# Kernel optimization log

Hardware: AMD Instinct MI355X
Metric: run time of the kernel (lower is better)

The kernel has to match this reference:

```python
import jax, jax.numpy as jnp
import numpy as np

# dims
N, T = 16, 2000            # batch, encoder frames
ENC, DEC = 512, 512        # enc_dim, dec_dim
ATT, C, K, H = 512, 10, 64, 4  # att_dim, conv_channels, loc_context, att_head


def setup_inputs() -> dict:
    key = jax.random.key(0)
    ks = jax.random.split(key, 16)
    s = 0.02
    enc_pad = jax.random.normal(ks[0], (N, T, ENC), jnp.float32)
    enc_len = jax.random.randint(ks[1], (N,), T // 2, T + 1, jnp.int32)
    dec_prev = jax.random.normal(ks[2], (N, DEC), jnp.float32)
    ali_prev = jax.random.uniform(ks[3], (N, H, T), jnp.float32)
    ali_prev = ali_prev / ali_prev.sum(-1, keepdims=True)
    # parameters (torch layout)
    We = jax.random.normal(ks[4], (ATT * H, ENC), jnp.float32) * s   # enc_proj weight
    be = jnp.zeros((ATT * H,), jnp.float32)                          # enc_proj bias
    Wk = jax.random.normal(ks[5], (ATT * H, ENC), jnp.float32) * s   # key_proj
    Wd = jax.random.normal(ks[6], (ATT * H, DEC), jnp.float32) * s   # dec_proj
    WF = jax.random.normal(ks[7], (C * H, 1, 2 * K + 1), jnp.float32) * s  # F: grouped conv1d
    bF = jnp.zeros((C * H,), jnp.float32)
    Wa = jax.random.normal(ks[8], (H, ATT, C), jnp.float32) * s      # att: 1x1 grouped conv, per-head [ATT,C]
    Ww = jax.random.normal(ks[9], (H, ATT), jnp.float32) * s         # w: 1x1 grouped conv, per-head [ATT]
    Wc = jax.random.normal(ks[10], (ENC, ATT * H), jnp.float32) * s  # ctx_proj
    bc = jnp.zeros((ENC,), jnp.float32)
    return {"enc_pad": enc_pad, "enc_len": enc_len, "dec_prev": dec_prev,
            "ali_prev": ali_prev, "We": We, "be": be, "Wk": Wk, "Wd": Wd,
            "WF": WF, "bF": bF, "Wa": Wa, "Ww": Ww, "Wc": Wc, "bc": bc}


def reference(enc_pad, enc_len, dec_prev, ali_prev, We, be, Wk, Wd, WF, bF, Wa, Ww, Wc, bc):
    n, t, _ = enc_pad.shape
    # enc_part: N x H x T x D
    ep = enc_pad @ We.T + be
    enc_part = ep.reshape(n, t, H, ATT).transpose(0, 2, 1, 3)
    # key_part: N x H x D x T (matches torch transpose(1,2).view ordering)
    kp = enc_pad @ Wk.T
    key_part = kp.transpose(0, 2, 1).reshape(n, H, ATT, t)
    # pad mask: N x T, True where padded
    pad_mask = jnp.arange(t)[None, :] >= enc_len[:, None]
    # location features: grouped conv1d over alignment, per head
    f = jax.lax.conv_general_dilated(
        ali_prev, WF, window_strides=(1,), padding=[(K, K)],
        dimension_numbers=("NCH", "OIH", "NCH"), feature_group_count=H)
    f = (f + bF[None, :, None]).reshape(n, H, C, t)
    # 1x1 grouped conv: C -> ATT per head
    att_part = jnp.einsum("hdc,nhct->nhdt", Wa, f)
    dec_part = (dec_prev @ Wd.T).reshape(n, H, ATT)
    sum_part = jnp.tanh(att_part + key_part + dec_part[..., None])  # N x H x D x T
    score = jnp.einsum("hd,nhdt->nht", Ww, sum_part)                # N x H x T
    score = jnp.where(pad_mask[:, None, :], -jnp.inf, score)
    ali = jax.nn.softmax(score, axis=-1)
    ctx = jnp.einsum("nht,nhtd->nhd", ali, enc_part).reshape(n, H * ATT)
    ctx = ctx @ Wc.T + bc
    return ali, ctx
```

## Files before the change

### kernel.cpp

```cpp
#include <hip/hip_runtime.h>

#define NB   16
#define TT   2000
#define TP   2048
#define SPT  2048
#define ENC  512
#define ATTD 512
#define HH   4
#define CC   10
#define KK   64
#define KW   129
#define HATT 2048

typedef unsigned short u16;
typedef __attribute__((ext_vector_type(8))) short bf16x8;
typedef __attribute__((ext_vector_type(4))) float f32x4;

#define AS1 __attribute__((address_space(1)))
#define AS3 __attribute__((address_space(3)))

#define CVT_BLOCKS   2176
#define CVT_THREADS  (CVT_BLOCKS * 256)

__device__ inline unsigned bfpack2(float lo, float hi) {
    unsigned a = __builtin_bit_cast(unsigned, lo);
    unsigned b = __builtin_bit_cast(unsigned, hi);
    a = (a + 0x7fffu + ((a >> 16) & 1u)) >> 16;
    b = (b + 0x7fffu + ((b >> 16) & 1u)) >> 16;
    return a | (b << 16);
}

__global__ __launch_bounds__(256) void prep_kernel(
    const float* __restrict__ enc, const float* __restrict__ Wk,
    const float* __restrict__ ali_prev, const float* __restrict__ WF,
    const float* __restrict__ bF, const float* __restrict__ dec_prev,
    const float* __restrict__ Wd, const float* __restrict__ Wa,
    const int* __restrict__ enc_len,
    u16* __restrict__ Abf, u16* __restrict__ Wkbf,
    u16* __restrict__ ftb, u16* __restrict__ wab,
    float* __restrict__ decp)
{
    __shared__ union {
        struct { float aliW[632]; float wfT[KW * CC]; float bfs[CC]; } cv;
        float dsl[16 * 128];
    } sm;
    const int bid = blockIdx.x, tid = threadIdx.x;

    if (bid < CVT_BLOCKS) {
        const long long ATOT = (long long)NB * TP * ENC;
        f32x4 v[4][2];
        bool live[4];
        long long g[4];
        #pragma unroll
        for (int it = 0; it < 4; it++) {
            long long cid = (long long)it * CVT_THREADS + bid * 256 + tid;
            long long gid = cid * 8;
            g[it] = gid;
            const float* s;
            bool valid = true;
            if (gid < ATOT) {
                int n = (int)(gid >> 20);
                int rem = (int)(gid & ((1 << 20) - 1));
                int r = rem >> 9, e = rem & 511;
                valid = (r < enc_len[n]);
                s = enc + ((long long)n * TT + r) * ENC + e;
            } else {
                s = Wk + (gid - ATOT);
            }
            live[it] = valid;
            if (valid) {
                v[it][0] = __builtin_nontemporal_load((const f32x4*)s);
                v[it][1] = __builtin_nontemporal_load((const f32x4*)s + 1);
            }
        }
        #pragma unroll
        for (int it = 0; it < 4; it++) {
            if (!live[it]) continue;
            uint4 out;
            out.x = bfpack2(v[it][0].x, v[it][0].y);
            out.y = bfpack2(v[it][0].z, v[it][0].w);
            out.z = bfpack2(v[it][1].x, v[it][1].y);
            out.w = bfpack2(v[it][1].z, v[it][1].w);
            if (g[it] < ATOT) *(uint4*)(Abf + g[it]) = out;
            else              *(uint4*)(Wkbf + (g[it] - ATOT)) = out;
        }
    } else if (bid < CVT_BLOCKS + 256) {
        int b2 = bid - CVT_BLOCKS;
        int tc = b2 & 3, h = (b2 >> 2) & 3, n = b2 >> 4;
        int t0 = tc * 500;
        float* aliW = sm.cv.aliW;
        float* wfT  = sm.cv.wfT;
        float* bfs  = sm.cv.bfs;
        const float* arow = ali_prev + ((long long)n * HH + h) * TT;
        for (int i = tid; i < 632; i += 256) {
            int tt = t0 - KK + i;
            aliW[i] = (tt >= 0 && tt < TT) ? arow[tt] : 0.f;
        }
        for (int i = tid; i < KW * CC; i += 256) {
            int k = i / CC, c = i - k * CC;
            wfT[i] = WF[(h * CC + c) * KW + k];
        }
        if (tid < CC) bfs[tid] = bF[h * CC + tid];
        __syncthreads();
        if (tid < 250) {
            float acc0[CC], acc1[CC];
            #pragma unroll
            for (int c = 0; c < CC; c++) { acc0[c] = 0.f; acc1[c] = 0.f; }
            const int base = 2 * tid;
            float2 w0 = *(const float2*)&aliW[base];
            for (int k = 0; k < 128; k += 2) {
                float2 w2 = *(const float2*)&aliW[base + k + 2];
                #pragma unroll
                for (int cj = 0; cj < 5; cj++) {
                    float2 fk  = *(const float2*)&wfT[k * CC + cj * 2];
                    float2 fk1 = *(const float2*)&wfT[(k + 1) * CC + cj * 2];
                    acc0[2*cj]   += w0.x * fk.x + w0.y * fk1.x;
                    acc0[2*cj+1] += w0.x * fk.y + w0.y * fk1.y;
                    acc1[2*cj]   += w0.y * fk.x + w2.x * fk1.x;
                    acc1[2*cj+1] += w0.y * fk.y + w2.x * fk1.y;
                }
                w0 = w2;
            }
            #pragma unroll
            for (int cj = 0; cj < 5; cj++) {
                float2 fk = *(const float2*)&wfT[128 * CC + cj * 2];
                acc0[2*cj]   += w0.x * fk.x;  acc0[2*cj+1] += w0.x * fk.y;
                acc1[2*cj]   += w0.y * fk.x;  acc1[2*cj+1] += w0.y * fk.y;
            }
            #pragma unroll
            for (int c = 0; c < CC; c++) { acc0[c] += bfs[c]; acc1[c] += bfs[c]; }
            int t = t0 + base;
            u16* frow = ftb + (((long long)(n * HH + h)) * TP + t) * 16;
            uint4 ra, rb;
            ra.x = bfpack2(acc0[0], acc0[1]); ra.y = bfpack2(acc0[2], acc0[3]);
            ra.z = bfpack2(acc0[4], acc0[5]); ra.w = bfpack2(acc0[6], acc0[7]);
            rb.x = bfpack2(acc0[8], acc0[9]); rb.y = 0u; rb.z = 0u; rb.w = 0u;
            *(uint4*)(frow)     = ra; *(uint4*)(frow + 8)  = rb;
            ra.x = bfpack2(acc1[0], acc1[1]); ra.y = bfpack2(acc1[2], acc1[3]);
            ra.z = bfpack2(acc1[4], acc1[5]); ra.w = bfpack2(acc1[6], acc1[7]);
            rb.x = bfpack2(acc1[8], acc1[9]);
            *(uint4*)(frow + 16) = ra; *(uint4*)(frow + 24) = rb;
        } else if (tc == 3) {
            uint4 z = {0u, 0u, 0u, 0u};
            int r0 = 2000 + (tid - 250) * 8;
            u16* frow = ftb + (((long long)(n * HH + h)) * TP + r0) * 16;
            for (int r = 0; r < 8; r++) {
                *(uint4*)(frow + r * 16)     = z;
                *(uint4*)(frow + r * 16 + 8) = z;
            }
        }
    } else if (bid < CVT_BLOCKS + 288) {
        int b2 = bid - (CVT_BLOCKS + 256);
        int kc = b2 >> 3, jc = b2 & 7;
        for (int i = tid; i < 2048; i += 256) {
            int nn = i >> 7, kk = i & 127;
            sm.dsl[i] = dec_prev[nn * 512 + kc * 128 + kk];
        }
        __syncthreads();
        int d = jc * 256 + tid;
        float acc[NB];
        #pragma unroll
        for (int n = 0; n < NB; n++) acc[n] = 0.f;
        const float4* w4 = (const float4*)(Wd + (long long)d * 512 + kc * 128);
        for (int e4 = 0; e4 < 32; e4++) {
            float4 w = w4[e4];
            #pragma unroll
            for (int n = 0; n < NB; n++) {
                const float* a = sm.dsl + n * 128 + e4 * 4;
                acc[n] += w.x * a[0] + w.y * a[1] + w.z * a[2] + w.w * a[3];
            }
        }
        #pragma unroll
        for (int n = 0; n < NB; n++) decp[((long long)kc * NB + n) * HATT + d] = acc[n];
    } else {
        int b2 = bid - (CVT_BLOCKS + 288);
        int j0 = b2 * 512 + tid * 2;
        #pragma unroll
        for (int q = 0; q < 2; q++) {
            int j = j0 + q;
            int hh = j >> 9, dd = j & 511;
            const float* wr = Wa + ((long long)(hh * ATTD + dd)) * CC;
            uint4 ra, rb;
            ra.x = bfpack2(wr[0], wr[1]); ra.y = bfpack2(wr[2], wr[3]);
            ra.z = bfpack2(wr[4], wr[5]); ra.w = bfpack2(wr[6], wr[7]);
            rb.x = bfpack2(wr[8], wr[9]); rb.y = 0u; rb.z = 0u; rb.w = 0u;
            u16* out = wab + (long long)j * 16;
            *(uint4*)(out)     = ra;
            *(uint4*)(out + 8) = rb;
        }
    }
}

__global__ __launch_bounds__(256, 4) void score_gemm_kernel(
    const u16* __restrict__ Abf, const u16* __restrict__ Bbf,
    const u16* __restrict__ ftb, const u16* __restrict__ wab,
    const float* __restrict__ decp, const float* __restrict__ Ww,
    const int* __restrict__ enc_len, float* __restrict__ score_part)
{
    __shared__ __attribute__((aligned(16))) char smem[32768];
    float* sred = (float*)smem;

    const int bid = blockIdx.x;
    const int xcd = bid & 7;
    const int lcl = bid >> 3;
    const int nt = lcl & 15;
    const int rr = lcl >> 4;
    const int n = rr >> 1, half = rr & 1;
    const int mtl = (xcd + n) & 7;
    const int mt = half ? (8 + mtl) : mtl;

    if (mt * 128 >= enc_len[n]) return;

    const int tid = threadIdx.x, wave = tid >> 6, lane = tid & 63;
    const int l16 = lane & 15, lk = lane >> 4;
    const int h = nt >> 2;

    const u16* Aptr = Abf + ((long long)n * TP + mt * 128) * ENC;
    const u16* Bptr = Bbf + (long long)nt * 128 * ENC;

    f32x4 acc[4][4];
    #pragma unroll
    for (int mi = 0; mi < 4; mi++)
        #pragma unroll
        for (int nj = 0; nj < 4; nj++) {
            f32x4 z = {0.f, 0.f, 0.f, 0.f};
            acc[mi][nj] = z;
        }

    const int wrow = (wave >> 1) * 64, wcol = (wave & 1) * 64;
    const int t0 = mt * 128, dd0 = (nt & 3) * 128;

    for (int kt = 0; kt < 8; kt++) {
        const int k0 = kt * 64;
        #pragma unroll
        for (int i = 0; i < 4; i++) {
            int b = i * 4096 + tid * 16;
            int r = b >> 7, kb = b & 127;
            int kbs = kb ^ ((r & 7) << 4);
            __builtin_amdgcn_global_load_lds(
                (const AS1 void*)(Aptr + r * ENC + k0 + (kbs >> 1)),
                (AS3 void*)(smem + i * 4096 + wave * 1024), 16, 0, 0);
            __builtin_amdgcn_global_load_lds(
                (const AS1 void*)(Bptr + r * ENC + k0 + (kbs >> 1)),
                (AS3 void*)(smem + 16384 + i * 4096 + wave * 1024), 16, 0, 0);
        }
        __syncthreads();
        #pragma unroll
        for (int ks = 0; ks < 64; ks += 32) {
            bf16x8 af[4], bf[4];
            #pragma unroll
            for (int mi = 0; mi < 4; mi++) {
                int row = wrow + mi * 16 + l16;
                int cb = (ks * 2 + lk * 16) ^ ((row & 7) << 4);
                af[mi] = *(const bf16x8*)(smem + row * 128 + cb);
            }
            #pragma unroll
            for (int nj = 0; nj < 4; nj++) {
                int row = wcol + nj * 16 + l16;
                int cb = (ks * 2 + lk * 16) ^ ((row & 7) << 4);
                bf[nj] = *(const bf16x8*)(smem + 16384 + row * 128 + cb);
            }
            #pragma unroll
            for (int mi = 0; mi < 4; mi++)
                #pragma unroll
                for (int nj = 0; nj < 4; nj++)
                    acc[mi][nj] = __builtin_amdgcn_mfma_f32_16x16x32_bf16(
                        af[mi], bf[nj], acc[mi][nj], 0, 0, 0);
        }
        __syncthreads();
    }

    {
        bf16x8 zer = {0, 0, 0, 0, 0, 0, 0, 0};
        bf16x8 af[4], bf[4];
        #pragma unroll
        for (int mi = 0; mi < 4; mi++) af[mi] = zer;
        #pragma unroll
        for (int nj = 0; nj < 4; nj++) bf[nj] = zer;
        if (lk < 2) {
            #pragma unroll
            for (int mi = 0; mi < 4; mi++)
                af[mi] = *(const bf16x8*)(ftb +
                    (((long long)(n * HH + h)) * TP + t0 + wrow + mi * 16 + l16) * 16 + lk * 8);
            #pragma unroll
            for (int nj = 0; nj < 4; nj++)
                bf[nj] = *(const bf16x8*)(wab +
                    ((long long)(nt * 128 + wcol + nj * 16 + l16)) * 16 + lk * 8);
        }
        #pragma unroll
        for (int mi = 0; mi < 4; mi++)
            #pragma unroll
            for (int nj = 0; nj < 4; nj++)
                acc[mi][nj] = __builtin_amdgcn_mfma_f32_16x16x32_bf16(
                    af[mi], bf[nj], acc[mi][nj], 0, 0, 0);
    }

    float wm2[4], dec4[4];
    #pragma unroll
    for (int nj = 0; nj < 4; nj++) {
        int cl = wcol + nj * 16 + l16;
        wm2[nj] = -2.f * Ww[h * ATTD + dd0 + cl];
        int j = nt * 128 + cl;
        dec4[nj] = decp[((long long)0 * NB + n) * HATT + j]
                 + decp[((long long)1 * NB + n) * HATT + j]
                 + decp[((long long)2 * NB + n) * HATT + j]
                 + decp[((long long)3 * NB + n) * HATT + j];
    }

    #pragma unroll
    for (int mi = 0; mi < 4; mi++) {
        #pragma unroll
        for (int j = 0; j < 4; j++) {
            int rl = wrow + mi * 16 + lk * 4 + j;
            float s = 0.f;
            #pragma unroll
            for (int nj = 0; nj < 4; nj++) {
                float v = acc[mi][nj][j] + dec4[nj];
                float e = __expf(v + v);
                s = fmaf(wm2[nj], __builtin_amdgcn_rcpf(e + 1.f), s);
            }
            s += __shfl_xor(s, 1); s += __shfl_xor(s, 2);
            s += __shfl_xor(s, 4); s += __shfl_xor(s, 8);
            if (l16 == 0) sred[(wave & 1) * 128 + rl] = s;
        }
    }
    __syncthreads();
    if (tid < 128) {
        int t = t0 + tid;
        if (t < TT)
            score_part[((long long)((nt & 3) * NB + n) * HH + h) * SPT + t] =
                sred[tid] + sred[128 + tid];
    }
}

__global__ __launch_bounds__(256) void smax_part_kernel(
    const float* __restrict__ score_part, const int* __restrict__ enc_len,
    float* __restrict__ mstat)
{
    int qr = blockIdx.x & 3, h = (blockIdx.x >> 2) & 3, n = blockIdx.x >> 4;
    int len = enc_len[n];
    int tid = threadIdx.x;
    int t = qr * 512 + tid * 2;
    float s0 = 0.f, s1 = 0.f;
    #pragma unroll
    for (int q = 0; q < 4; q++) {
        float2 sv = *(const float2*)(score_part +
            (((long long)(q * NB + n)) * HH + h) * SPT + t);
        s0 += sv.x; s1 += sv.y;
    }
    bool v0 = (t < len), v1 = (t + 1 < len);
    float lmax = -3.4e38f;
    if (v0) lmax = s0;
    if (v1) lmax = fmaxf(lmax, s1);
    __shared__ float red[256];
    red[tid] = lmax; __syncthreads();
    for (int off = 128; off; off >>= 1) {
        if (tid < off) red[tid] = fmaxf(red[tid], red[tid + off]);
        __syncthreads();
    }
    float bmax = red[0];
    __syncthreads();
    float lsum = 0.f;
    if (v0) lsum += expf(s0 - bmax);
    if (v1) lsum += expf(s1 - bmax);
    red[tid] = lsum; __syncthreads();
    for (int off = 128; off; off >>= 1) {
        if (tid < off) red[tid] += red[tid + off];
        __syncthreads();
    }
    if (tid == 0) {
        float2 o = {bmax, red[0]};
        *(float2*)(mstat + ((n * HH + h) * 4 + qr) * 2) = o;
    }
}

__global__ __launch_bounds__(256) void a_enc_kernel(
    const float* __restrict__ score_part, const float* __restrict__ mstat,
    const u16* __restrict__ Abf, const int* __restrict__ enc_len,
    float* __restrict__ aep, float* __restrict__ ali)
{
    int tc = blockIdx.x & 31, n = blockIdx.x >> 5;
    int tid = threadIdx.x;
    int len = enc_len[n];
    int tbeg = tc * 63;
    int cnt = len - tbeg; if (cnt > 63) cnt = 63; if (cnt < 0) cnt = 0;
    __shared__ float aliS[HH][64];
    __shared__ float red[2][4][129];
    {
        int hh = tid >> 6, tt = tid & 63;
        int t = tbeg + tt;
        const float2* ms = (const float2*)(mstat) + (n * HH + hh) * 4;
        float2 p0 = ms[0], p1 = ms[1], p2 = ms[2], p3 = ms[3];
        float gm = fmaxf(fmaxf(p0.x, p1.x), fmaxf(p2.x, p3.x));
        float gs = p0.y * expf(p0.x - gm) + p1.y * expf(p1.x - gm)
                 + p2.y * expf(p2.x - gm) + p3.y * expf(p3.x - gm);
        float gi = 1.f / gs;
        float av = 0.f;
        if (tt < cnt) {
            float s = 0.f;
            #pragma unroll
            for (int q = 0; q < 4; q++)
                s += score_part[(((long long)(q * NB + n)) * HH + hh) * SPT + t];
            av = expf(s - gm) * gi;
        }
        aliS[hh][tt] = av;
        if (tt < 63 && t < TT)
            ali[((long long)n * HH + hh) * TT + t] = av;
    }
    __syncthreads();
    const int l = tid & 127, tq = tid >> 7;
    float acc[HH][4];
    #pragma unroll
    for (int hh = 0; hh < HH; hh++)
        #pragma unroll
        for (int k = 0; k < 4; k++) acc[hh][k] = 0.f;
    #pragma unroll 4
    for (int ii = 0; ii < 32; ii++) {
        int tl = ii * 2 + tq;
        if (tl < cnt) {
            uint2 u = *(const uint2*)(Abf + ((long long)n * TP + tbeg + tl) * ENC + l * 4);
            float e0 = __builtin_bit_cast(float, u.x << 16);
            float e1 = __builtin_bit_cast(float, u.x & 0xffff0000u);
            float e2 = __builtin_bit_cast(float, u.y << 16);
            float e3 = __builtin_bit_cast(float, u.y & 0xffff0000u);
            #pragma unroll
            for (int hh = 0; hh < HH; hh++) {
                float w = aliS[hh][tl];
                acc[hh][0] += w * e0; acc[hh][1] += w * e1;
                acc[hh][2] += w * e2; acc[hh][3] += w * e3;
            }
        }
    }
    #pragma unroll
    for (int hh = 0; hh < HH; hh++) {
        __syncthreads();
        #pragma unroll
        for (int k = 0; k < 4; k++) red[tq][k][l] = acc[hh][k];
        __syncthreads();
        int d2 = tid * 2;
        float v0 = red[0][d2 & 3][d2 >> 2] + red[1][d2 & 3][d2 >> 2];
        int d3 = d2 + 1;
        float v1 = red[0][d3 & 3][d3 >> 2] + red[1][d3 & 3][d3 >> 2];
        float2 o = {v0, v1};
        *(float2*)(aep + (((long long)tc * NB + n) * HH + hh) * ENC + d2) = o;
    }
}

__global__ __launch_bounds__(256) void reduce1_kernel(
    const float* __restrict__ aep, float* __restrict__ aep2)
{
    int i = blockIdx.x * 256 + threadIdx.x;
    float s = 0.f;
    for (int tc = 0; tc < 32; tc++)
        s += aep[(long long)tc * 32768 + i];
    aep2[i] = s;
}

__global__ __launch_bounds__(256) void ctx_tmp_kernel(
    const float* __restrict__ aep2, const float* __restrict__ We,
    const float* __restrict__ be, float* __restrict__ ctmp)
{
    int kc = blockIdx.x >> 5, jc = blockIdx.x & 31;
    int tid = threadIdx.x;
    int h = (jc * 64) >> 9;
    __shared__ float aes[16 * 64];
    for (int i = tid; i < 1024; i += 256) {
        int nn = i >> 6, kk = i & 63;
        aes[i] = aep2[(nn * HH + h) * ENC + kc * 64 + kk];
    }
    __syncthreads();
    int j = jc * 64 + (tid & 63);
    int ng = tid >> 6;
    float acc[4];
    #pragma unroll
    for (int n2 = 0; n2 < 4; n2++) acc[n2] = 0.f;
    const float4* w4 = (const float4*)(We + (long long)j * 512 + kc * 64);
    for (int e4 = 0; e4 < 16; e4++) {
        float4 w = w4[e4];
        #pragma unroll
        for (int n2 = 0; n2 < 4; n2++) {
            const float* a = aes + (ng * 4 + n2) * 64 + e4 * 4;
            acc[n2] += w.x * a[0] + w.y * a[1] + w.z * a[2] + w.w * a[3];
        }
    }
    float bias = (kc == 0) ? be[j] : 0.f;
    #pragma unroll
    for (int n2 = 0; n2 < 4; n2++)
        ctmp[((long long)kc * NB + ng * 4 + n2) * HATT + j] = acc[n2] + bias;
}

__global__ __launch_bounds__(256) void reduce2_kernel(
    const float* __restrict__ ctmp, float* __restrict__ ctmp2)
{
    int i = blockIdx.x * 256 + threadIdx.x;
    float s = 0.f;
    #pragma unroll
    for (int kc = 0; kc < 8; kc++)
        s += ctmp[(long long)kc * 32768 + i];
    ctmp2[i] = s;
}

__global__ __launch_bounds__(256) void ctx_out_kernel(
    const float* __restrict__ ctmp2, const float* __restrict__ Wc,
    const float* __restrict__ bc, float* __restrict__ out_ctx)
{
    int ec = blockIdx.x & 31, nc = blockIdx.x >> 5;
    int tid = threadIdx.x;
    __shared__ float ct[4 * 2048];
    __shared__ float red[16][4][17];
    for (int i = tid; i < 4 * 2048; i += 256) {
        int nn = i >> 11, j = i & 2047;
        ct[i] = ctmp2[(nc * 4 + nn) * HATT + j];
    }
    __syncthreads();
    int eo = tid & 15, kq = tid >> 4;
    int eg = ec * 16 + eo;
    float acc[4];
    #pragma unroll
    for (int nn = 0; nn < 4; nn++) acc[nn] = 0.f;
    const float4* w4 = (const float4*)(Wc + (long long)eg * HATT + kq * 128);
    for (int j4 = 0; j4 < 32; j4++) {
        float4 w = w4[j4];
        #pragma unroll
        for (int nn = 0; nn < 4; nn++) {
            const float* a = ct + nn * 2048 + kq * 128 + j4 * 4;
            acc[nn] += w.x * a[0] + w.y * a[1] + w.z * a[2] + w.w * a[3];
        }
    }
    #pragma unroll
    for (int nn = 0; nn < 4; nn++) red[kq][nn][eo] = acc[nn];
    __syncthreads();
    if (tid < 64) {
        int eo2 = tid & 15, nn2 = tid >> 4;
        float s = 0.f;
        #pragma unroll
        for (int kq2 = 0; kq2 < 16; kq2++) s += red[kq2][nn2][eo2];
        out_ctx[((long long)(nc * 4 + nn2)) * 512 + ec * 16 + eo2] = s + bc[ec * 16 + eo2];
    }
}

extern "C" void kernel_launch(void* const* d_in, const int* in_sizes, int n_in,
                              void* d_out, int out_size, void* d_ws, size_t ws_size,
                              hipStream_t stream)
{
    (void)in_sizes; (void)n_in; (void)out_size; (void)ws_size;
    const float* enc_pad  = (const float*)d_in[0];
    const int*   enc_len  = (const int*)  d_in[1];
    const float* dec_prev = (const float*)d_in[2];
    const float* ali_prev = (const float*)d_in[3];
    const float* We = (const float*)d_in[4];
    const float* be = (const float*)d_in[5];
    const float* Wk = (const float*)d_in[6];
    const float* Wd = (const float*)d_in[7];
    const float* WF = (const float*)d_in[8];
    const float* bF = (const float*)d_in[9];
    const float* Wa = (const float*)d_in[10];
    const float* Ww = (const float*)d_in[11];
    const float* Wc = (const float*)d_in[12];
    const float* bc = (const float*)d_in[13];

    char* ws = (char*)d_ws;
    u16*   Abf  = (u16*)  (ws);
    u16*   Wkbf = (u16*)  (ws + 33554432);
    u16*   ftb  = (u16*)  (ws + 35651584);
    u16*   wab  = (u16*)  (ws + 39845888);
    float* decp = (float*)(ws + 39911424);
    float* spart= (float*)(ws + 40435712);
    float* aep  = (float*)(ws + 35651584);
    float* mstat= (float*)(ws + 39845888);
    float* aep2 = (float*)(ws + 39911424);
    float* ctmp = (float*)(ws + 40435712);
    float* ctmp2= (float*)(ws + 33554432);

    float* ali = (float*)d_out;
    float* ctx = (float*)d_out + NB * HH * TT;

    prep_kernel      <<<2468, 256, 0, stream>>>(enc_pad, Wk, ali_prev, WF, bF,
                                                dec_prev, Wd, Wa, enc_len,
                                                Abf, Wkbf, ftb, wab, decp);
    score_gemm_kernel<<<4096, 256, 0, stream>>>(Abf, Wkbf, ftb, wab, decp, Ww,
                                                enc_len, spart);
    smax_part_kernel <<<256,  256, 0, stream>>>(spart, enc_len, mstat);
    a_enc_kernel     <<<512,  256, 0, stream>>>(spart, mstat, Abf, enc_len,
                                                aep, ali);
    reduce1_kernel   <<<128,  256, 0, stream>>>(aep, aep2);
    ctx_tmp_kernel   <<<256,  256, 0, stream>>>(aep2, We, be, ctmp);
    reduce2_kernel   <<<128,  256, 0, stream>>>(ctmp, ctmp2);
    ctx_out_kernel   <<<128,  256, 0, stream>>>(ctmp2, Wc, bc, ctx);
}
```

Before: 158.6 us.

## Make score GEMM loop over four tiles per block; cache summed scores

The score GEMM launch goes from 4096 blocks to 1024, and each block now loops over four tile assignments (blockIdx + it*1024) while keeping the same XCD/tile mapping. This cuts block launch and tail overhead and lets blocks whose tiles are fully masked move on to the next tile. The softmax partial kernel also writes the summed four-quarter scores to a scratch buffer, so a_enc reads one value instead of four partials. Risks are a lower number of resident waves hiding latency, load imbalance because the skipped masked tiles are spread unevenly across blocks, and a scratch buffer that aliases aep2's workspace region.

```diff
diff --git a/kernel.cpp b/kernel.cpp
--- a/kernel.cpp
+++ b/kernel.cpp
@@ -200,142 +200,145 @@
     __shared__ __attribute__((aligned(16))) char smem[32768];
     float* sred = (float*)smem;
 
-    const int bid = blockIdx.x;
-    const int xcd = bid & 7;
-    const int lcl = bid >> 3;
-    const int nt = lcl & 15;
-    const int rr = lcl >> 4;
-    const int n = rr >> 1, half = rr & 1;
-    const int mtl = (xcd + n) & 7;
-    const int mt = half ? (8 + mtl) : mtl;
-
-    if (mt * 128 >= enc_len[n]) return;
-
     const int tid = threadIdx.x, wave = tid >> 6, lane = tid & 63;
     const int l16 = lane & 15, lk = lane >> 4;
-    const int h = nt >> 2;
-
-    const u16* Aptr = Abf + ((long long)n * TP + mt * 128) * ENC;
-    const u16* Bptr = Bbf + (long long)nt * 128 * ENC;
-
-    f32x4 acc[4][4];
-    #pragma unroll
-    for (int mi = 0; mi < 4; mi++)
-        #pragma unroll
-        for (int nj = 0; nj < 4; nj++) {
-            f32x4 z = {0.f, 0.f, 0.f, 0.f};
-            acc[mi][nj] = z;
-        }
-
     const int wrow = (wave >> 1) * 64, wcol = (wave & 1) * 64;
-    const int t0 = mt * 128, dd0 = (nt & 3) * 128;
-
-    for (int kt = 0; kt < 8; kt++) {
-        const int k0 = kt * 64;
-        #pragma unroll
-        for (int i = 0; i < 4; i++) {
-            int b = i * 4096 + tid * 16;
-            int r = b >> 7, kb = b & 127;
-            int kbs = kb ^ ((r & 7) << 4);
-            __builtin_amdgcn_global_load_lds(
-                (const AS1 void*)(Aptr + r * ENC + k0 + (kbs >> 1)),
-                (AS3 void*)(smem + i * 4096 + wave * 1024), 16, 0, 0);
-            __builtin_amdgcn_global_load_lds(
-                (const AS1 void*)(Bptr + r * ENC + k0 + (kbs >> 1)),
-                (AS3 void*)(smem + 16384 + i * 4096 + wave * 1024), 16, 0, 0);
-        }
-        __syncthreads();
-        #pragma unroll
-        for (int ks = 0; ks < 64; ks += 32) {
-            bf16x8 af[4], bf[4];
+
+    for (int it = 0; it < 4; it++) {
+        const int lbid = blockIdx.x + it * 1024;
+        const int xcd = lbid & 7;
+        const int lcl = lbid >> 3;
+        const int nt = lcl & 15;
+        const int rr = lcl >> 4;
+        const int n = rr >> 1, half = rr & 1;
+        const int mtl = (xcd + n) & 7;
+        const int mt = half ? (8 + mtl) : mtl;
+
+        if (mt * 128 < enc_len[n]) {
+            const int h = nt >> 2;
+            const u16* Aptr = Abf + ((long long)n * TP + mt * 128) * ENC;
+            const u16* Bptr = Bbf + (long long)nt * 128 * ENC;
+
+            f32x4 acc[4][4];
+            #pragma unroll
+            for (int mi = 0; mi < 4; mi++)
+                #pragma unroll
+                for (int nj = 0; nj < 4; nj++) {
+                    f32x4 z = {0.f, 0.f, 0.f, 0.f};
+                    acc[mi][nj] = z;
+                }
+
+            const int t0 = mt * 128, dd0 = (nt & 3) * 128;
+
+            for (int kt = 0; kt < 8; kt++) {
+                const int k0 = kt * 64;
+                #pragma unroll
+                for (int i = 0; i < 4; i++) {
+                    int b = i * 4096 + tid * 16;
+                    int r = b >> 7, kb = b & 127;
+                    int kbs = kb ^ ((r & 7) << 4);
+                    __builtin_amdgcn_global_load_lds(
+                        (const AS1 void*)(Aptr + r * ENC + k0 + (kbs >> 1)),
+                        (AS3 void*)(smem + i * 4096 + wave * 1024), 16, 0, 0);
+                    __builtin_amdgcn_global_load_lds(
+                        (const AS1 void*)(Bptr + r * ENC + k0 + (kbs >> 1)),
+                        (AS3 void*)(smem + 16384 + i * 4096 + wave * 1024), 16, 0, 0);
+                }
+                __syncthreads();
+                #pragma unroll
+                for (int ks = 0; ks < 64; ks += 32) {
+                    bf16x8 af[4], bf[4];
+                    #pragma unroll
+                    for (int mi = 0; mi < 4; mi++) {
+                        int row = wrow + mi * 16 + l16;
+                        int cb = (ks * 2 + lk * 16) ^ ((row & 7) << 4);
+                        af[mi] = *(const bf16x8*)(smem + row * 128 + cb);
+                    }
+                    #pragma unroll
+                    for (int nj = 0; nj < 4; nj++) {
+                        int row = wcol + nj * 16 + l16;
+                        int cb = (ks * 2 + lk * 16) ^ ((row & 7) << 4);
+                        bf[nj] = *(const bf16x8*)(smem + 16384 + row * 128 + cb);
+                    }
+                    #pragma unroll
+                    for (int mi = 0; mi < 4; mi++)
+                        #pragma unroll
+                        for (int nj = 0; nj < 4; nj++)
+                            acc[mi][nj] = __builtin_amdgcn_mfma_f32_16x16x32_bf16(
+                                af[mi], bf[nj], acc[mi][nj], 0, 0, 0);
+                }
+                __syncthreads();
+            }
+
+            {
+                bf16x8 zer = {0, 0, 0, 0, 0, 0, 0, 0};
+                bf16x8 af[4], bf[4];
+                #pragma unroll
+                for (int mi = 0; mi < 4; mi++) af[mi] = zer;
+                #pragma unroll
+                for (int nj = 0; nj < 4; nj++) bf[nj] = zer;
+                if (lk < 2) {
+                    #pragma unroll
+                    for (int mi = 0; mi < 4; mi++)
+                        af[mi] = *(const bf16x8*)(ftb +
+                            (((long long)(n * HH + h)) * TP + t0 + wrow + mi * 16 + l16) * 16 + lk * 8);
+                    #pragma unroll
+                    for (int nj = 0; nj < 4; nj++)
+                        bf[nj] = *(const bf16x8*)(wab +
+                            ((long long)(nt * 128 + wcol + nj * 16 + l16)) * 16 + lk * 8);
+                }
+                #pragma unroll
+                for (int mi = 0; mi < 4; mi++)
+                    #pragma unroll
+                    for (int nj = 0; nj < 4; nj++)
+                        acc[mi][nj] = __builtin_amdgcn_mfma_f32_16x16x32_bf16(
+                            af[mi], bf[nj], acc[mi][nj], 0, 0, 0);
+            }
+
+            float wm2[4], dec4[4];
+            #pragma unroll
+            for (int nj = 0; nj < 4; nj++) {
+                int cl = wcol + nj * 16 + l16;
+                wm2[nj] = -2.f * Ww[h * ATTD + dd0 + cl];
+                int j = nt * 128 + cl;
+                dec4[nj] = decp[((long long)0 * NB + n) * HATT + j]
+                         + decp[((long long)1 * NB + n) * HATT + j]
+                         + decp[((long long)2 * NB + n) * HATT + j]
+                         + decp[((long long)3 * NB + n) * HATT + j];
+            }
+
             #pragma unroll
             for (int mi = 0; mi < 4; mi++) {
-                int row = wrow + mi * 16 + l16;
-                int cb = (ks * 2 + lk * 16) ^ ((row & 7) << 4);
-                af[mi] = *(const bf16x8*)(smem + row * 128 + cb);
-            }
-            #pragma unroll
-            for (int nj = 0; nj < 4; nj++) {
-                int row = wcol + nj * 16 + l16;
-                int cb = (ks * 2 + lk * 16) ^ ((row & 7) << 4);
-                bf[nj] = *(const bf16x8*)(smem + 16384 + row * 128 + cb);
-            }
-            #pragma unroll
-            for (int mi = 0; mi < 4; mi++)
-                #pragma unroll
-                for (int nj = 0; nj < 4; nj++)
-                    acc[mi][nj] = __builtin_amdgcn_mfma_f32_16x16x32_bf16(
-                        af[mi], bf[nj], acc[mi][nj], 0, 0, 0);
-        }
-        __syncthreads();
-    }
-
-    {
-        bf16x8 zer = {0, 0, 0, 0, 0, 0, 0, 0};
-        bf16x8 af[4], bf[4];
-        #pragma unroll
-        for (int mi = 0; mi < 4; mi++) af[mi] = zer;
-        #pragma unroll
-        for (int nj = 0; nj < 4; nj++) bf[nj] = zer;
-        if (lk < 2) {
-            #pragma unroll
-            for (int mi = 0; mi < 4; mi++)
-                af[mi] = *(const bf16x8*)(ftb +
-                    (((long long)(n * HH + h)) * TP + t0 + wrow + mi * 16 + l16) * 16 + lk * 8);
-            #pragma unroll
-            for (int nj = 0; nj < 4; nj++)
-                bf[nj] = *(const bf16x8*)(wab +
-                    ((long long)(nt * 128 + wcol + nj * 16 + l16)) * 16 + lk * 8);
-        }
-        #pragma unroll
-        for (int mi = 0; mi < 4; mi++)
-            #pragma unroll
-            for (int nj = 0; nj < 4; nj++)
-                acc[mi][nj] = __builtin_amdgcn_mfma_f32_16x16x32_bf16(
-                    af[mi], bf[nj], acc[mi][nj], 0, 0, 0);
-    }
-
-    float wm2[4], dec4[4];
-    #pragma unroll
-    for (int nj = 0; nj < 4; nj++) {
-        int cl = wcol + nj * 16 + l16;
-        wm2[nj] = -2.f * Ww[h * ATTD + dd0 + cl];
-        int j = nt * 128 + cl;
-        dec4[nj] = decp[((long long)0 * NB + n) * HATT + j]
-                 + decp[((long long)1 * NB + n) * HATT + j]
-                 + decp[((long long)2 * NB + n) * HATT + j]
-                 + decp[((long long)3 * NB + n) * HATT + j];
-    }
-
-    #pragma unroll
-    for (int mi = 0; mi < 4; mi++) {
-        #pragma unroll
-        for (int j = 0; j < 4; j++) {
-            int rl = wrow + mi * 16 + lk * 4 + j;
-            float s = 0.f;
-            #pragma unroll
-            for (int nj = 0; nj < 4; nj++) {
-                float v = acc[mi][nj][j] + dec4[nj];
-                float e = __expf(v + v);
-                s = fmaf(wm2[nj], __builtin_amdgcn_rcpf(e + 1.f), s);
-            }
-            s += __shfl_xor(s, 1); s += __shfl_xor(s, 2);
-            s += __shfl_xor(s, 4); s += __shfl_xor(s, 8);
-            if (l16 == 0) sred[(wave & 1) * 128 + rl] = s;
-        }
-    }
-    __syncthreads();
-    if (tid < 128) {
-        int t = t0 + tid;
-        if (t < TT)
-            score_part[((long long)((nt & 3) * NB + n) * HH + h) * SPT + t] =
-                sred[tid] + sred[128 + tid];
+                #pragma unroll
+                for (int j = 0; j < 4; j++) {
+                    int rl = wrow + mi * 16 + lk * 4 + j;
+                    float s = 0.f;
+                    #pragma unroll
+                    for (int nj = 0; nj < 4; nj++) {
+                        float v = acc[mi][nj][j] + dec4[nj];
+                        float e = __expf(v + v);
+                        s = fmaf(wm2[nj], __builtin_amdgcn_rcpf(e + 1.f), s);
+                    }
+                    s += __shfl_xor(s, 1); s += __shfl_xor(s, 2);
+                    s += __shfl_xor(s, 4); s += __shfl_xor(s, 8);
+                    if (l16 == 0) sred[(wave & 1) * 128 + rl] = s;
+                }
+            }
+            __syncthreads();
+            if (tid < 128) {
+                int t = t0 + tid;
+                if (t < TT)
+                    score_part[((long long)((nt & 3) * NB + n) * HH + h) * SPT + t] =
+                        sred[tid] + sred[128 + tid];
+            }
+        }
+        __syncthreads();
     }
 }
 
 __global__ __launch_bounds__(256) void smax_part_kernel(
     const float* __restrict__ score_part, const int* __restrict__ enc_len,
-    float* __restrict__ mstat)
+    float* __restrict__ mstat, float* __restrict__ scr)
 {
     int qr = blockIdx.x & 3, h = (blockIdx.x >> 2) & 3, n = blockIdx.x >> 4;
     int len = enc_len[n];
@@ -347,6 +350,10 @@
         float2 sv = *(const float2*)(score_part +
             (((long long)(q * NB + n)) * HH + h) * SPT + t);
         s0 += sv.x; s1 += sv.y;
+    }
+    {
+        float2 o = {s0, s1};
+        *(float2*)(scr + (n * HH + h) * SPT + t) = o;
     }
     bool v0 = (t < len), v1 = (t + 1 < len);
     float lmax = -3.4e38f;
@@ -375,7 +382,7 @@
 }
 
 __global__ __launch_bounds__(256) void a_enc_kernel(
-    const float* __restrict__ score_part, const float* __restrict__ mstat,
+    const float* __restrict__ scr, const float* __restrict__ mstat,
     const u16* __restrict__ Abf, const int* __restrict__ enc_len,
     float* __restrict__ aep, float* __restrict__ ali)
 {
@@ -397,10 +404,7 @@
         float gi = 1.f / gs;
         float av = 0.f;
         if (tt < cnt) {
-            float s = 0.f;
-            #pragma unroll
-            for (int q = 0; q < 4; q++)
-                s += score_part[(((long long)(q * NB + n)) * HH + hh) * SPT + t];
+            float s = scr[(n * HH + hh) * SPT + t];
             av = expf(s - gm) * gi;
         }
         aliS[hh][tt] = av;
@@ -568,6 +572,7 @@
     float* spart= (float*)(ws + 40435712);
     float* aep  = (float*)(ws + 35651584);
     float* mstat= (float*)(ws + 39845888);
+    float* scr  = (float*)(ws + 39911424);
     float* aep2 = (float*)(ws + 39911424);
     float* ctmp = (float*)(ws + 40435712);
     float* ctmp2= (float*)(ws + 33554432);
@@ -578,10 +583,10 @@
     prep_kernel      <<<2468, 256, 0, stream>>>(enc_pad, Wk, ali_prev, WF, bF,
                                                 dec_prev, Wd, Wa, enc_len,
                                                 Abf, Wkbf, ftb, wab, decp);
-    score_gemm_kernel<<<4096, 256, 0, stream>>>(Abf, Wkbf, ftb, wab, decp, Ww,
+    score_gemm_kernel<<<1024, 256, 0, stream>>>(Abf, Wkbf, ftb, wab, decp, Ww,
                                                 enc_len, spart);
-    smax_part_kernel <<<256,  256, 0, stream>>>(spart, enc_len, mstat);
-    a_enc_kernel     <<<512,  256, 0, stream>>>(spart, mstat, Abf, enc_len,
+    smax_part_kernel <<<256,  256, 0, stream>>>(spart, enc_len, mstat, scr);
+    a_enc_kernel     <<<512,  256, 0, stream>>>(scr, mstat, Abf, enc_len,
                                                 aep, ali);
     reduce1_kernel   <<<128,  256, 0, stream>>>(aep, aep2);
     ctx_tmp_kernel   <<<256,  256, 0, stream>>>(aep2, We, be, ctmp);
```

Result: slower. 223.6 us (+41.0%).
